# Performance work log

Hardware: AMD Instinct MI355X
Metric: run time of the kernel (lower is better)

Reference implementation:

```python
import jax, jax.numpy as jnp
import numpy as np
import math

B, C, N, T = 8, 128, 256, 64  # batch, d_model, nodes, timesteps
H = 8                          # attention heads
NUM_STEPS = 50                 # diffusion steps


def _conv2d(x, w, b):
    # Conv2d with kernel (1,3), padding (0,1); x: (B,C,N,T), w: (O,I,1,3)
    y = jax.lax.conv_general_dilated(x, w, (1, 1), [(0, 0), (1, 1)],
                                     dimension_numbers=('NCHW', 'OIHW', 'NCHW'))
    return y + b[None, :, None, None]


def _linear(x, w, b=None):
    y = jnp.einsum('...i,oi->...o', x, w)
    return y if b is None else y + b


def _ln(x, g, b, eps=1e-5):
    m = jnp.mean(x, -1, keepdims=True)
    v = jnp.var(x, -1, keepdims=True)
    return (x - m) * jax.lax.rsqrt(v + eps) * g + b


def _forward(step, x, adj, wq, bq, wk, bk, w1, b1, w2, b2, theta,
             ln0_g, ln0_b, ln1_g, ln1_b, p1_w, p1_b, p2_w, p2_b,
             dxc_w, dxc_b, dec_w, dec_b, dc1_w, dc1_b, dp2_w, dp2_b):
    dk = C // H
    sq = 1.0 / math.sqrt(dk)
    sc = 1.0 / math.sqrt(C)
    # ---- normalized graph Laplacian: D^{-1/2} A D^{-1/2} (get_laplacian, normalize=True)
    d = jnp.sum(adj, -1) ** -0.5
    Lap = adj * d[:, None] * d[None, :]  # (N,N)
    # ---- temporal attention with conv-derived Q/K (MultiHeadAttentionAwareTemporal)
    q = _conv2d(x, wq, bq).reshape(B, H, dk, N, T).transpose(0, 3, 1, 4, 2)  # (B,N,H,T,dk)
    k = _conv2d(x, wk, bk).reshape(B, H, dk, N, T).transpose(0, 3, 1, 4, 2)
    v = _linear(x.transpose(0, 2, 3, 1), w1, b1).reshape(B, N, T, H, dk).transpose(0, 1, 3, 2, 4)
    p = jax.nn.softmax(jnp.einsum('bnhtd,bnhsd->bnhts', q, k) * sq, axis=-1)
    o = jnp.einsum('bnhts,bnhsd->bnhtd', p, v).transpose(0, 1, 3, 2, 4).reshape(B, N, T, C)
    xp = x.transpose(0, 2, 3, 1) + _ln(_linear(o, w2, b2), ln0_g, ln0_b)  # (B,N,T,C)
    # ---- spatial attention GCN (Spatial_Attention_layer + spatialAttentionGCN)
    xt = xp.transpose(0, 2, 1, 3)  # (B,T,N,C)
    sat = jax.nn.softmax(jnp.einsum('btnf,btmf->btnm', xt, xt) * sc, axis=-1) * sc
    y = jnp.einsum('btnm,btmf->btnf', Lap[None, None] * sat, xt)
    y = jax.nn.relu(_linear(y, theta)).transpose(0, 2, 1, 3)  # (B,N,T,C)
    h = xp + _ln(y, ln1_g, ln1_b)
    # ---- diffusion step embedding (DiffusionEmbedding)
    dim = C // 2
    freqs = 10.0 ** (jnp.arange(dim, dtype=jnp.float32) / (dim - 1) * 4.0)
    tab = jnp.arange(NUM_STEPS, dtype=jnp.float32)[:, None] * freqs[None, :]
    tab = jnp.concatenate([jnp.sin(tab), jnp.cos(tab)], -1)  # (NUM_STEPS, C)
    e = jax.nn.silu(_linear(tab[step], p1_w, p1_b))
    e = jax.nn.silu(_linear(e, p2_w, p2_b))  # (B,C)
    h = h + e[:, None, None, :]
    # ---- Decoder: conv + sigmoid-gated add + relu + 1x1 projection to 2 channels
    enc = h.transpose(0, 3, 1, 2)  # (B,C,N,T)
    xh = _conv2d(enc, dxc_w, dxc_b)
    ec = _conv2d(enc, dec_w, dec_b)
    out = jax.nn.relu(xh + jax.nn.sigmoid(ec) + _conv2d(ec, dc1_w, dc1_b))
    out = jnp.einsum('bcnt,oc->bont', out, dp2_w) + dp2_b[None, :, None, None]  # (B,2,N,T)
    return out


def setup_inputs() -> dict:
    key = jax.random.key(0)
    ks = iter(jax.random.split(key, 40))
    s = 1.0 / math.sqrt(C)
    sk = 1.0 / math.sqrt(3 * C)

    def nrm(shape, scale):
        return jax.random.normal(next(ks), shape, jnp.float32) * scale

    return {
        'x': nrm((B, C, N, T), 1.0),
        'adj': jax.random.uniform(next(ks), (N, N), jnp.float32, 0.1, 1.0),
        'step': jax.random.randint(next(ks), (B,), 0, NUM_STEPS, jnp.int32),
        'wq': nrm((C, C, 1, 3), sk), 'bq': jnp.zeros((C,), jnp.float32),
        'wk': nrm((C, C, 1, 3), sk), 'bk': jnp.zeros((C,), jnp.float32),
        'w1': nrm((C, C), s), 'b1': jnp.zeros((C,), jnp.float32),
        'w2': nrm((C, C), s), 'b2': jnp.zeros((C,), jnp.float32),
        'theta': nrm((C, C), s),
        'ln0_g': jnp.ones((C,), jnp.float32), 'ln0_b': jnp.zeros((C,), jnp.float32),
        'ln1_g': jnp.ones((C,), jnp.float32), 'ln1_b': jnp.zeros((C,), jnp.float32),
        'p1_w': nrm((C, C), s), 'p1_b': jnp.zeros((C,), jnp.float32),
        'p2_w': nrm((C, C), s), 'p2_b': jnp.zeros((C,), jnp.float32),
        'dxc_w': nrm((C, C, 1, 3), sk), 'dxc_b': jnp.zeros((C,), jnp.float32),
        'dec_w': nrm((C, C, 1, 3), sk), 'dec_b': jnp.zeros((C,), jnp.float32),
        'dc1_w': nrm((C, C, 1, 3), sk), 'dc1_b': jnp.zeros((C,), jnp.float32),
        'dp2_w': nrm((2, C), s), 'dp2_b': jnp.zeros((2,), jnp.float32),
    }


def reference(x, adj, step, wq, bq, wk, bk, w1, b1, w2, b2, theta,
              ln0_g, ln0_b, ln1_g, ln1_b, p1_w, p1_b, p2_w, p2_b,
              dxc_w, dxc_b, dec_w, dec_b, dc1_w, dc1_b, dp2_w, dp2_b):
    return _forward(step, x, adj, wq, bq, wk, bk, w1, b1, w2, b2, theta,
                    ln0_g, ln0_b, ln1_g, ln1_b, p1_w, p1_b, p2_w, p2_b,
                    dxc_w, dxc_b, dec_w, dec_b, dc1_w, dc1_b, dp2_w, dp2_b)
```

## Files before the change

### kernel.cpp

```cpp
#include <hip/hip_runtime.h>
#include <hip/hip_bf16.h>

namespace {

constexpr int C = 128, N = 256, T = 64, Bsz = 8;
constexpr int TILE = T * C;
constexpr size_t BIGE = (size_t)Bsz * N * T * C;

typedef short v8s __attribute__((ext_vector_type(8)));
typedef float v4f __attribute__((ext_vector_type(4)));

__device__ __forceinline__ float bfu(unsigned short u) {
  unsigned int x = ((unsigned int)u) << 16;
  return __uint_as_float(x);
}
__device__ __forceinline__ unsigned short f2b(float v) {
  __hip_bfloat16 h = __float2bfloat16(v);
  return *(unsigned short*)&h;
}
__device__ __forceinline__ unsigned int pk2(float a, float b) {
  return (unsigned int)f2b(a) | ((unsigned int)f2b(b) << 16);
}
__device__ __forceinline__ float ld(const void* p, size_t i, int f32) {
  if (f32) return ((const float*)p)[i];
  return bfu(((const unsigned short*)p)[i]);
}
__device__ __forceinline__ float sigm(float x) { return 1.f / (1.f + __expf(-x)); }

__global__ __launch_bounds__(64) void k_sniff(const unsigned short* x, int* flag) {
  __shared__ int cnt[64];
  int tid = threadIdx.x;
  int c = 0;
  for (int u = 0; u < 8; ++u) {
    unsigned short v = x[tid * 8 + u];
    int e = (v >> 7) & 255;
    c += (e >= 97 && e <= 157) ? 1 : 0;
  }
  cnt[tid] = c;
  __syncthreads();
  if (tid == 0) {
    int s = 0;
    for (int i = 0; i < 64; ++i) s += cnt[i];
    flag[0] = (s < 435) ? 1 : 0;
  }
}

__global__ __launch_bounds__(256) void k_dsh(const void* adj, const int* flag, float* dsh) {
  int f = flag[0];
  int row = blockIdx.x * 8 + (threadIdx.x >> 5);
  int l32 = threadIdx.x & 31;
  float s = 0.f;
#pragma unroll
  for (int j = 0; j < 8; ++j) s += ld(adj, (size_t)row * 256 + l32 + j * 32, f);
#pragma unroll
  for (int m = 16; m > 0; m >>= 1) s += __shfl_xor(s, m, 32);
  if (l32 == 0) dsh[row] = 1.f / sqrtf(s);
}

struct PrepArgs {
  const int* flag;
  const void *wq, *wk, *w1, *w2, *th, *dxc, *dec, *dc1;
  const void *bq, *bk, *b1, *b2, *l0g, *l0b, *l1g, *l1b, *dxcb, *decb, *dc1b, *dp2w, *dp2b;
  unsigned short *wqkB, *w1B, *w2B;
  __hip_bfloat16* thB;
  unsigned short *decWb, *dxcWb, *dc1Wb;
  float *bqk, *b1f, *b2f, *l0gf, *l0bf, *l1gf, *l1bf, *dxcbf, *decbf, *dc1bf, *dp2wf, *dp2bf;
};

__global__ __launch_bounds__(256) void k_prepall(
    PrepArgs a, const void* adj, const float* dsh, float* lap, const int* step,
    const void* p1w, const void* p1b, const void* p2w, const void* p2b, float* e) {
  __shared__ float sh[256];
  __shared__ float e1[128];
  int f = a.flag[0];
  int blk = blockIdx.x, tid = threadIdx.x;
  if (blk < 128) {
    int idx = blk * 256 + tid;
    const int stride = 32768;
    for (int i = idx; i < 256 * 384; i += stride) {
      int o = i / 384, k = i - o * 384;
      int j = k >> 7, ii = k & 127;
      float v = (o < 128) ? ld(a.wq, (o * 128 + ii) * 3 + j, f)
                          : ld(a.wk, ((o - 128) * 128 + ii) * 3 + j, f);
      a.wqkB[i] = f2b(v);
    }
    for (int i = idx; i < 16384; i += stride) {
      a.w1B[i] = f2b(ld(a.w1, i, f));
      a.w2B[i] = f2b(ld(a.w2, i, f));
      a.thB[i] = __float2bfloat16(ld(a.th, i, f));
    }
    for (int i = idx; i < 16384; i += stride) {
      int o = i >> 7, ii = i & 127;
      int sbase = (o * 128 + ii) * 3;
#pragma unroll
      for (int j = 0; j < 3; ++j) {
        int dsti = o * 384 + j * 128 + ii;
        a.decWb[dsti] = f2b(ld(a.dec, sbase + j, f));
        a.dxcWb[dsti] = f2b(ld(a.dxc, sbase + j, f));
        a.dc1Wb[dsti] = f2b(ld(a.dc1, sbase + j, f));
      }
    }
    for (int i = idx; i < 256; i += stride) {
      a.bqk[i] = (i < 128) ? ld(a.bq, i, f) : ld(a.bk, i - 128, f);
      a.dp2wf[i] = ld(a.dp2w, i, f);
    }
    for (int i = idx; i < 128; i += stride) {
      a.b1f[i] = ld(a.b1, i, f);   a.b2f[i] = ld(a.b2, i, f);
      a.l0gf[i] = ld(a.l0g, i, f); a.l0bf[i] = ld(a.l0b, i, f);
      a.l1gf[i] = ld(a.l1g, i, f); a.l1bf[i] = ld(a.l1b, i, f);
      a.dxcbf[i] = ld(a.dxcb, i, f); a.decbf[i] = ld(a.decb, i, f); a.dc1bf[i] = ld(a.dc1b, i, f);
    }
    if (idx < 2) a.dp2bf[idx] = ld(a.dp2b, idx, f);
  } else if (blk < 192) {
    int n0 = (blk - 128) * 4;
    for (int idx = tid; idx < 1024; idx += 256) {
      int n = n0 + (idx >> 8), m = idx & 255;
      lap[n * 256 + m] = ld(adj, n * 256 + m, f) * dsh[n] * dsh[m];
    }
  } else {
    int b = blk - 192;
    if (tid < 128) {
      float sv = (float)step[b];
      int i0 = tid & 63;
      float fr = powf(10.f, (float)i0 / 63.f * 4.f);
      float ang = sv * fr;
      sh[tid] = (tid < 64) ? sinf(ang) : cosf(ang);
    }
    __syncthreads();
    if (tid < 128) {
      float aa = ld(p1b, tid, f);
      for (int i = 0; i < 128; ++i) aa += sh[i] * ld(p1w, tid * 128 + i, f);
      aa = aa * sigm(aa);
      e1[tid] = aa;
    }
    __syncthreads();
    if (tid < 128) {
      float a2 = ld(p2b, tid, f);
      for (int i = 0; i < 128; ++i) a2 += e1[i] * ld(p2w, tid * 128 + i, f);
      e[b * 128 + tid] = a2 * sigm(a2);
    }
  }
}

constexpr int XBS = 136;
constexpr int VTS = 72;

__global__ __launch_bounds__(512, 4) void k_mega1(
    const void* xin, const int* flag,
    const unsigned short* wqkB, const float* bqk,
    const unsigned short* w1B, const float* b1f,
    const unsigned short* w2B, const float* b2f,
    const float* l0g, const float* l0b, float* g0) {
  int bn = blockIdx.x, b = bn >> 8, n = bn & 255;
  __shared__ unsigned short Xb[66 * XBS];
  __shared__ unsigned short qo[64 * XBS];
  __shared__ unsigned short kls[64 * XBS];
  __shared__ unsigned short vT[128 * VTS];
  __shared__ float pS[8 * 64], pQ[8 * 64];
  __shared__ float mrow[64], vrow[64];
  int tid = threadIdx.x;
  int wv = tid >> 6, lane = tid & 63, quad = lane >> 4, lr = lane & 15;
  int f = flag[0];
  int hb = wv * 16;
  const v8s zz = {0, 0, 0, 0, 0, 0, 0, 0};
  {
    size_t xoff = (size_t)b * C * N * T + (size_t)n * T;
    const int NT = N * T;
    for (int idx = tid; idx < 1024; idx += 512) {
      int t = idx & 63, c0 = (idx >> 6) * 8;
      union { unsigned short us[8]; uint4 q; } pk;
      if (f) {
        const float* xp = (const float*)xin + xoff + (size_t)c0 * NT + t;
#pragma unroll
        for (int u = 0; u < 8; ++u) pk.us[u] = f2b(xp[(size_t)u * NT]);
      } else {
        const unsigned short* xp = (const unsigned short*)xin + xoff + (size_t)c0 * NT + t;
#pragma unroll
        for (int u = 0; u < 8; ++u) pk.us[u] = xp[(size_t)u * NT];
      }
      *(uint4*)&Xb[(t + 1) * XBS + c0] = pk.q;
    }
    if (tid < 128) { Xb[tid] = 0; Xb[65 * XBS + tid] = 0; }
  }
  __syncthreads();
  {
    int mt0 = wv * 2;
    v4f acc[2][4];
#pragma unroll
    for (int mi = 0; mi < 2; ++mi)
#pragma unroll
      for (int nt = 0; nt < 4; ++nt) acc[mi][nt] = (v4f){0.f, 0.f, 0.f, 0.f};
    for (int j = 0; j < 3; ++j) {
#pragma unroll
      for (int kt = 0; kt < 4; ++kt) {
        int ko = j * 128 + kt * 32 + quad * 8;
        v8s a0 = *(const v8s*)&wqkB[(mt0 * 16 + lr) * 384 + ko];
        v8s a1 = *(const v8s*)&wqkB[((mt0 + 1) * 16 + lr) * 384 + ko];
        int bko = kt * 32 + quad * 8;
#pragma unroll
        for (int nt = 0; nt < 4; ++nt) {
          v8s bb = *(const v8s*)&Xb[(nt * 16 + lr + j) * XBS + bko];
          acc[0][nt] = __builtin_amdgcn_mfma_f32_16x16x32_bf16(a0, bb, acc[0][nt], 0, 0, 0);
          acc[1][nt] = __builtin_amdgcn_mfma_f32_16x16x32_bf16(a1, bb, acc[1][nt], 0, 0, 0);
        }
      }
    }
    unsigned short* dst = (wv < 4) ? qo : kls;
#pragma unroll
    for (int mi = 0; mi < 2; ++mi) {
      int og = (mt0 + mi) * 16 + quad * 4;
      int oo = og & 127;
#pragma unroll
      for (int nt = 0; nt < 4; ++nt) {
        int t = nt * 16 + lr;
        *(unsigned int*)&dst[t * XBS + oo] =
            pk2(acc[mi][nt][0] + bqk[og], acc[mi][nt][1] + bqk[og + 1]);
        *(unsigned int*)&dst[t * XBS + oo + 2] =
            pk2(acc[mi][nt][2] + bqk[og + 2], acc[mi][nt][3] + bqk[og + 3]);
      }
    }
  }
  {
    v4f av[4];
#pragma unroll
    for (int nt = 0; nt < 4; ++nt) av[nt] = (v4f){0.f, 0.f, 0.f, 0.f};
#pragma unroll
    for (int kt = 0; kt < 4; ++kt) {
      int ko = kt * 32 + quad * 8;
      v8s a = *(const v8s*)&w1B[(wv * 16 + lr) * 128 + ko];
#pragma unroll
      for (int nt = 0; nt < 4; ++nt) {
        v8s bb = *(const v8s*)&Xb[(nt * 16 + lr + 1) * XBS + ko];
        av[nt] = __builtin_amdgcn_mfma_f32_16x16x32_bf16(a, bb, av[nt], 0, 0, 0);
      }
    }
#pragma unroll
    for (int nt = 0; nt < 4; ++nt) {
      int t = nt * 16 + lr;
#pragma unroll
      for (int r = 0; r < 4; ++r) {
        int o = hb + quad * 4 + r;
        vT[o * VTS + t] = f2b(av[nt][r] + b1f[o]);
      }
    }
  }
  __syncthreads();
  {
    v4f sa[4][4];
#pragma unroll
    for (int ms = 0; ms < 4; ++ms)
#pragma unroll
      for (int nt = 0; nt < 4; ++nt) sa[ms][nt] = (v4f){0.f, 0.f, 0.f, 0.f};
    {
      v8s afs[4], bfs[4];
#pragma unroll
      for (int ms = 0; ms < 4; ++ms)
        afs[ms] = (quad < 2) ? *(const v8s*)&kls[(ms * 16 + lr) * XBS + hb + quad * 8] : zz;
#pragma unroll
      for (int nt = 0; nt < 4; ++nt)
        bfs[nt] = (quad < 2) ? *(const v8s*)&qo[(nt * 16 + lr) * XBS + hb + quad * 8] : zz;
#pragma unroll
      for (int ms = 0; ms < 4; ++ms)
#pragma unroll
        for (int nt = 0; nt < 4; ++nt)
          sa[ms][nt] = __builtin_amdgcn_mfma_f32_16x16x32_bf16(afs[ms], bfs[nt], sa[ms][nt], 0, 0, 0);
    }
#pragma unroll
    for (int nt = 0; nt < 4; ++nt) {
      float mx = -1e30f;
#pragma unroll
      for (int ms = 0; ms < 4; ++ms)
#pragma unroll
        for (int r = 0; r < 4; ++r) {
          float v = sa[ms][nt][r] * 0.25f;
          sa[ms][nt][r] = v;
          mx = fmaxf(mx, v);
        }
      mx = fmaxf(mx, __shfl_xor(mx, 16, 64));
      mx = fmaxf(mx, __shfl_xor(mx, 32, 64));
      float ssum = 0.f;
#pragma unroll
      for (int ms = 0; ms < 4; ++ms)
#pragma unroll
        for (int r = 0; r < 4; ++r) {
          float e = __expf(sa[ms][nt][r] - mx);
          sa[ms][nt][r] = e;
          ssum += e;
        }
      ssum += __shfl_xor(ssum, 16, 64);
      ssum += __shfl_xor(ssum, 32, 64);
      float inv = 1.f / ssum;
#pragma unroll
      for (int ms = 0; ms < 4; ++ms)
#pragma unroll
        for (int r = 0; r < 4; ++r) sa[ms][nt][r] *= inv;
    }
    v4f ov[4];
#pragma unroll
    for (int nt = 0; nt < 4; ++nt) ov[nt] = (v4f){0.f, 0.f, 0.f, 0.f};
#pragma unroll
    for (int kt = 0; kt < 2; ++kt) {
      unsigned int pA[4][2], pB[4][2];
#pragma unroll
      for (int nt = 0; nt < 4; ++nt) {
#pragma unroll
        for (int h = 0; h < 2; ++h) {
          pA[nt][h] = pk2(sa[2 * kt][nt][2 * h], sa[2 * kt][nt][2 * h + 1]);
          pB[nt][h] = pk2(sa[2 * kt + 1][nt][2 * h], sa[2 * kt + 1][nt][2 * h + 1]);
        }
      }
      v8s aV = *(const v8s*)&vT[(hb + lr) * VTS + kt * 32 + quad * 8];
#pragma unroll
      for (int nt = 0; nt < 4; ++nt) {
        union { unsigned int u[4]; v8s s; } bu;
#pragma unroll
        for (int w = 0; w < 4; ++w) {
          int src = (2 * (quad & 1) + (w >> 1)) * 16 + lr;
          unsigned int x0 = (unsigned int)__shfl((int)pA[nt][w & 1], src, 64);
          unsigned int x1 = (unsigned int)__shfl((int)pB[nt][w & 1], src, 64);
          bu.u[w] = (quad >> 1) ? x1 : x0;
        }
        ov[nt] = __builtin_amdgcn_mfma_f32_16x16x32_bf16(aV, bu.s, ov[nt], 0, 0, 0);
      }
    }
#pragma unroll
    for (int nt = 0; nt < 4; ++nt) {
      int t = nt * 16 + lr;
      *(unsigned int*)&qo[t * XBS + hb + quad * 4] = pk2(ov[nt][0], ov[nt][1]);
      *(unsigned int*)&qo[t * XBS + hb + quad * 4 + 2] = pk2(ov[nt][2], ov[nt][3]);
    }
  }
  __syncthreads();
  v4f aw[4];
  {
#pragma unroll
    for (int nt = 0; nt < 4; ++nt) aw[nt] = (v4f){0.f, 0.f, 0.f, 0.f};
#pragma unroll
    for (int kt = 0; kt < 4; ++kt) {
      int ko = kt * 32 + quad * 8;
      v8s a = *(const v8s*)&w2B[(wv * 16 + lr) * 128 + ko];
#pragma unroll
      for (int nt = 0; nt < 4; ++nt) {
        v8s bb = *(const v8s*)&qo[(nt * 16 + lr) * XBS + ko];
        aw[nt] = __builtin_amdgcn_mfma_f32_16x16x32_bf16(a, bb, aw[nt], 0, 0, 0);
      }
    }
    int ob = hb + quad * 4;
#pragma unroll
    for (int nt = 0; nt < 4; ++nt) {
      float s = 0.f, q2 = 0.f;
#pragma unroll
      for (int r = 0; r < 4; ++r) {
        aw[nt][r] += b2f[ob + r];
        s += aw[nt][r];
        q2 += aw[nt][r] * aw[nt][r];
      }
      s += __shfl_xor(s, 16, 64);  s += __shfl_xor(s, 32, 64);
      q2 += __shfl_xor(q2, 16, 64); q2 += __shfl_xor(q2, 32, 64);
      if (quad == 0) {
        pS[wv * 64 + nt * 16 + lr] = s;
        pQ[wv * 64 + nt * 16 + lr] = q2;
      }
    }
  }
  __syncthreads();
  if (tid < 64) {
    float s = 0.f, q2 = 0.f;
#pragma unroll
    for (int w = 0; w < 8; ++w) { s += pS[w * 64 + tid]; q2 += pQ[w * 64 + tid]; }
    float mm = s * (1.f / 128.f);
    mrow[tid] = mm;
    vrow[tid] = rsqrtf(q2 * (1.f / 128.f) - mm * mm + 1e-5f);
  }
  __syncthreads();
  {
    int ob = hb + quad * 4;
    float gg[4], bb2[4];
#pragma unroll
    for (int r = 0; r < 4; ++r) { gg[r] = l0g[ob + r]; bb2[r] = l0b[ob + r]; }
    float* dst = g0 + (size_t)bn * TILE;
#pragma unroll
    for (int nt = 0; nt < 4; ++nt) {
      int t = nt * 16 + lr;
      float m = mrow[t], rs = vrow[t];
      ushort4 xr = *(const ushort4*)&Xb[(t + 1) * XBS + ob];
      float4 o4;
      o4.x = (aw[nt][0] - m) * rs * gg[0] + bb2[0] + bfu(xr.x);
      o4.y = (aw[nt][1] - m) * rs * gg[1] + bb2[1] + bfu(xr.y);
      o4.z = (aw[nt][2] - m) * rs * gg[2] + bb2[2] + bfu(xr.z);
      o4.w = (aw[nt][3] - m) * rs * gg[3] + bb2[3] + bfu(xr.w);
      *(float4*)&dst[t * 128 + ob] = o4;
    }
  }
}

constexpr int XS = 136;
constexpr int TS = 264;

__global__ __launch_bounds__(512, 1) void k_megasp(
    const float* g0, const float* lap, const unsigned short* thB,
    const float* l1g, const float* l1b, const float* e, unsigned short* g0b) {
  int bt = blockIdx.x, b = bt >> 6, t = bt & 63;
  __shared__ unsigned short R1[256 * XS];
  __shared__ unsigned short R2[256 * XS];
  unsigned short* Xhi = R1;
  unsigned short* Xlo = R2;
  unsigned short* Xt = R2;
  unsigned short* Pld = R1;
  int tid = threadIdx.x;
  int wv = tid >> 6, lane = tid & 63, quad = lane >> 4, lr = lane & 15;
  int wrow0 = wv * 32;
  const float sc = 0.08838834764831845f;
  {
    size_t base = (size_t)b * (N * (size_t)TILE) + (size_t)t * 128;
    for (int idx = tid * 4; idx < 32768; idx += 2048) {
      int n = idx >> 7, c = idx & 127;
      float4 v4 = *(const float4*)&g0[base + (size_t)n * TILE + c];
      ushort4 h, l;
      h.x = f2b(v4.x); l.x = f2b(v4.x - bfu(h.x));
      h.y = f2b(v4.y); l.y = f2b(v4.y - bfu(h.y));
      h.z = f2b(v4.z); l.z = f2b(v4.z - bfu(h.z));
      h.w = f2b(v4.w); l.w = f2b(v4.w - bfu(h.w));
      *(ushort4*)&Xhi[n * XS + c] = h;
      *(ushort4*)&Xlo[n * XS + c] = l;
    }
  }
  __syncthreads();
  v4f acc[2][16];
#pragma unroll
  for (int mi = 0; mi < 2; ++mi)
#pragma unroll
    for (int nt = 0; nt < 16; ++nt) acc[mi][nt] = (v4f){0.f, 0.f, 0.f, 0.f};
  for (int kt = 0; kt < 4; ++kt) {
    int ko = kt * 32 + quad * 8;
    v8s ah0 = *(const v8s*)&Xhi[(wrow0 + lr) * XS + ko];
    v8s al0 = *(const v8s*)&Xlo[(wrow0 + lr) * XS + ko];
    v8s ah1 = *(const v8s*)&Xhi[(wrow0 + 16 + lr) * XS + ko];
    v8s al1 = *(const v8s*)&Xlo[(wrow0 + 16 + lr) * XS + ko];
#pragma unroll
    for (int nt = 0; nt < 16; ++nt) {
      v8s bh = *(const v8s*)&Xhi[(nt * 16 + lr) * XS + ko];
      v8s bl = *(const v8s*)&Xlo[(nt * 16 + lr) * XS + ko];
      acc[0][nt] = __builtin_amdgcn_mfma_f32_16x16x32_bf16(ah0, bh, acc[0][nt], 0, 0, 0);
      acc[0][nt] = __builtin_amdgcn_mfma_f32_16x16x32_bf16(ah0, bl, acc[0][nt], 0, 0, 0);
      acc[0][nt] = __builtin_amdgcn_mfma_f32_16x16x32_bf16(al0, bh, acc[0][nt], 0, 0, 0);
      acc[1][nt] = __builtin_amdgcn_mfma_f32_16x16x32_bf16(ah1, bh, acc[1][nt], 0, 0, 0);
      acc[1][nt] = __builtin_amdgcn_mfma_f32_16x16x32_bf16(ah1, bl, acc[1][nt], 0, 0, 0);
      acc[1][nt] = __builtin_amdgcn_mfma_f32_16x16x32_bf16(al1, bh, acc[1][nt], 0, 0, 0);
    }
  }
  __syncthreads();
  for (int task = tid; task < 8192; task += 512) {
    int c = task & 127, n0 = (task >> 7) * 4;
    ushort4 w;
    w.x = Xhi[(n0 + 0) * XS + c];
    w.y = Xhi[(n0 + 1) * XS + c];
    w.z = Xhi[(n0 + 2) * XS + c];
    w.w = Xhi[(n0 + 3) * XS + c];
    *(ushort4*)&Xt[c * TS + n0] = w;
  }
  __syncthreads();
  unsigned int pk1[2][8][2];
#pragma unroll
  for (int mi = 0; mi < 2; ++mi) {
#pragma unroll
    for (int r = 0; r < 4; ++r) {
      int row = wrow0 + 16 * mi + quad * 4 + r;
      float mx = -1e30f;
#pragma unroll
      for (int nt = 0; nt < 16; ++nt) {
        acc[mi][nt][r] *= sc;
        mx = fmaxf(mx, acc[mi][nt][r]);
      }
#pragma unroll
      for (int m = 8; m > 0; m >>= 1) mx = fmaxf(mx, __shfl_xor(mx, m, 16));
      float ex[16];
      float ssum = 0.f;
#pragma unroll
      for (int nt = 0; nt < 16; ++nt) { ex[nt] = __expf(acc[mi][nt][r] - mx); ssum += ex[nt]; }
#pragma unroll
      for (int m = 8; m > 0; m >>= 1) ssum += __shfl_xor(ssum, m, 16);
      float inv = sc / ssum;
      const float* lrow = lap + row * 256 + lr;
#pragma unroll
      for (int nt = 0; nt < 8; ++nt)
        Pld[row * XS + nt * 16 + lr] = f2b(ex[nt] * inv * lrow[nt * 16]);
#pragma unroll
      for (int nt = 8; nt < 16; ++nt) {
        unsigned int hbw = (unsigned int)f2b(ex[nt] * inv * lrow[nt * 16]);
        if ((r & 1) == 0) pk1[mi][nt - 8][r >> 1] = hbw;
        else pk1[mi][nt - 8][r >> 1] |= hbw << 16;
      }
    }
  }
  v4f acc2[2][8];
#pragma unroll
  for (int mi = 0; mi < 2; ++mi)
#pragma unroll
    for (int nt = 0; nt < 8; ++nt) acc2[mi][nt] = (v4f){0.f, 0.f, 0.f, 0.f};
#pragma unroll
  for (int h = 0; h < 2; ++h) {
    if (h == 1) {
#pragma unroll
      for (int mi = 0; mi < 2; ++mi) {
        int rowb = wrow0 + 16 * mi + quad * 4;
#pragma unroll
        for (int k = 0; k < 8; ++k) {
          int col = k * 16 + lr;
          unsigned int u0 = pk1[mi][k][0], u1 = pk1[mi][k][1];
          Pld[(rowb + 0) * XS + col] = (unsigned short)u0;
          Pld[(rowb + 1) * XS + col] = (unsigned short)(u0 >> 16);
          Pld[(rowb + 2) * XS + col] = (unsigned short)u1;
          Pld[(rowb + 3) * XS + col] = (unsigned short)(u1 >> 16);
        }
      }
    }
    for (int kt = 0; kt < 4; ++kt) {
      int ko = kt * 32 + quad * 8;
      v8s pa0 = *(const v8s*)&Pld[(wrow0 + lr) * XS + ko];
      v8s pa1 = *(const v8s*)&Pld[(wrow0 + 16 + lr) * XS + ko];
#pragma unroll
      for (int nt = 0; nt < 8; ++nt) {
        v8s xb = *(const v8s*)&Xt[(nt * 16 + lr) * TS + h * 128 + ko];
        acc2[0][nt] = __builtin_amdgcn_mfma_f32_16x16x32_bf16(pa0, xb, acc2[0][nt], 0, 0, 0);
        acc2[1][nt] = __builtin_amdgcn_mfma_f32_16x16x32_bf16(pa1, xb, acc2[1][nt], 0, 0, 0);
      }
    }
  }
  __syncthreads();
  unsigned short* yB = R2;
  unsigned short* ths = R1;
#pragma unroll
  for (int mi = 0; mi < 2; ++mi) {
    int nb = wrow0 + 16 * mi + quad * 4;
#pragma unroll
    for (int nt = 0; nt < 8; ++nt) {
      int c = nt * 16 + lr;
#pragma unroll
      for (int r = 0; r < 4; ++r)
        yB[(nb + r) * XS + c] = f2b(acc2[mi][nt][r]);
    }
  }
  for (int idx = tid * 8; idx < 16384; idx += 4096) {
    int o = idx >> 7, k = idx & 127;
    *(uint4*)&ths[o * 136 + k] = *(const uint4*)&thB[idx];
  }
  __syncthreads();
  v4f acc3[2][8];
#pragma unroll
  for (int nt2 = 0; nt2 < 2; ++nt2)
#pragma unroll
    for (int ot = 0; ot < 8; ++ot) acc3[nt2][ot] = (v4f){0.f, 0.f, 0.f, 0.f};
#pragma unroll
  for (int kt = 0; kt < 4; ++kt) {
    int ko = kt * 32 + quad * 8;
    v8s b0 = *(const v8s*)&yB[((wv * 2 + 0) * 16 + lr) * XS + ko];
    v8s b1 = *(const v8s*)&yB[((wv * 2 + 1) * 16 + lr) * XS + ko];
#pragma unroll
    for (int ot = 0; ot < 8; ++ot) {
      v8s a = *(const v8s*)&ths[(ot * 16 + lr) * 136 + ko];
      acc3[0][ot] = __builtin_amdgcn_mfma_f32_16x16x32_bf16(a, b0, acc3[0][ot], 0, 0, 0);
      acc3[1][ot] = __builtin_amdgcn_mfma_f32_16x16x32_bf16(a, b1, acc3[1][ot], 0, 0, 0);
    }
  }
  float mmv[2], rrv[2];
#pragma unroll
  for (int nt2 = 0; nt2 < 2; ++nt2) {
    float s = 0.f, q2 = 0.f;
#pragma unroll
    for (int ot = 0; ot < 8; ++ot)
#pragma unroll
      for (int r = 0; r < 4; ++r) {
        float v = fmaxf(acc3[nt2][ot][r], 0.f);
        acc3[nt2][ot][r] = v;
        s += v; q2 += v * v;
      }
    s += __shfl_xor(s, 16, 64);  s += __shfl_xor(s, 32, 64);
    q2 += __shfl_xor(q2, 16, 64); q2 += __shfl_xor(q2, 32, 64);
    mmv[nt2] = s * (1.f / 128.f);
    rrv[nt2] = rsqrtf(q2 * (1.f / 128.f) - mmv[nt2] * mmv[nt2] + 1e-5f);
  }
  {
    const float* eb = e + b * 128;
#pragma unroll
    for (int ot = 0; ot < 8; ++ot) {
      int o0 = ot * 16 + quad * 4;
      float gg[4], bb2[4], ev[4];
#pragma unroll
      for (int r = 0; r < 4; ++r) { gg[r] = l1g[o0 + r]; bb2[r] = l1b[o0 + r]; ev[r] = eb[o0 + r]; }
#pragma unroll
      for (int nt2 = 0; nt2 < 2; ++nt2) {
        int n = (wv * 2 + nt2) * 16 + lr;
        float m = mmv[nt2], rs = rrv[nt2];
        size_t ga = ((size_t)(b * 256 + n)) * TILE + (size_t)t * 128 + o0;
        float4 xa = *(const float4*)&g0[ga];
        ushort4 pk;
        pk.x = f2b((acc3[nt2][ot][0] - m) * rs * gg[0] + bb2[0] + xa.x + ev[0]);
        pk.y = f2b((acc3[nt2][ot][1] - m) * rs * gg[1] + bb2[1] + xa.y + ev[1]);
        pk.z = f2b((acc3[nt2][ot][2] - m) * rs * gg[2] + bb2[2] + xa.z + ev[2]);
        pk.w = f2b((acc3[nt2][ot][3] - m) * rs * gg[3] + bb2[3] + xa.w + ev[3]);
        *(ushort4*)&g0b[ga] = pk;
      }
    }
  }
}

__global__ __launch_bounds__(512, 4) void k_megadec(
    const unsigned short* g0b, const unsigned short* decW, const float* decb,
    const unsigned short* dxcW, const float* dxcb,
    const unsigned short* dc1W, const float* dc1b,
    const float* dp2w, const float* dp2b, const int* flag, void* outv) {
  int bn = blockIdx.x, b = bn >> 8, n = bn & 255;
  int f32o = flag[0];
  __shared__ unsigned short Xm[66 * XBS];
  __shared__ unsigned short E2[66 * XBS];
  __shared__ float pb0[8][64], pb1[8][64];
  int tid = threadIdx.x;
  int wv = tid >> 6, lane = tid & 63, quad = lane >> 4, lr = lane & 15;
  int m0 = wv * 16;
  const unsigned short* gp = g0b + (size_t)bn * TILE;
  for (int idx = tid * 8; idx < TILE; idx += 4096) {
    int t = idx >> 7, c = idx & 127;
    *(uint4*)&Xm[(t + 1) * XBS + c] = *(const uint4*)&gp[idx];
  }
  if (tid < 128) {
    Xm[tid] = 0; Xm[65 * XBS + tid] = 0;
    E2[tid] = 0; E2[65 * XBS + tid] = 0;
  }
  __syncthreads();
  v4f acc[4];
  float ecv[4][4];
#pragma unroll
  for (int nt = 0; nt < 4; ++nt) acc[nt] = (v4f){0.f, 0.f, 0.f, 0.f};
  for (int j = 0; j < 3; ++j) {
#pragma unroll
    for (int kt = 0; kt < 4; ++kt) {
      v8s a = *(const v8s*)&decW[(m0 + lr) * 384 + j * 128 + kt * 32 + quad * 8];
      int bko = kt * 32 + quad * 8;
#pragma unroll
      for (int nt = 0; nt < 4; ++nt) {
        v8s bb = *(const v8s*)&Xm[(nt * 16 + lr + j) * XBS + bko];
        acc[nt] = __builtin_amdgcn_mfma_f32_16x16x32_bf16(a, bb, acc[nt], 0, 0, 0);
      }
    }
  }
#pragma unroll
  for (int nt = 0; nt < 4; ++nt) {
    int t = nt * 16 + lr;
    int o = m0 + quad * 4;
    ushort4 pk;
#pragma unroll
    for (int r = 0; r < 4; ++r) {
      float v = acc[nt][r] + decb[o + r];
      ecv[nt][r] = v;
      ((unsigned short*)&pk)[r] = f2b(v);
    }
    *(ushort4*)&E2[(t + 1) * XBS + o] = pk;
  }
  __syncthreads();
  v4f ax[4], ac[4];
#pragma unroll
  for (int nt = 0; nt < 4; ++nt) { ax[nt] = (v4f){0.f,0.f,0.f,0.f}; ac[nt] = (v4f){0.f,0.f,0.f,0.f}; }
  for (int j = 0; j < 3; ++j) {
#pragma unroll
    for (int kt = 0; kt < 4; ++kt) {
      int wo = (m0 + lr) * 384 + j * 128 + kt * 32 + quad * 8;
      v8s a1 = *(const v8s*)&dxcW[wo];
      v8s a2 = *(const v8s*)&dc1W[wo];
      int bko = kt * 32 + quad * 8;
#pragma unroll
      for (int nt = 0; nt < 4; ++nt) {
        int row = (nt * 16 + lr + j) * XBS + bko;
        v8s b1 = *(const v8s*)&Xm[row];
        v8s b2v = *(const v8s*)&E2[row];
        ax[nt] = __builtin_amdgcn_mfma_f32_16x16x32_bf16(a1, b1, ax[nt], 0, 0, 0);
        ac[nt] = __builtin_amdgcn_mfma_f32_16x16x32_bf16(a2, b2v, ac[nt], 0, 0, 0);
      }
    }
  }
#pragma unroll
  for (int nt = 0; nt < 4; ++nt) {
    float p0 = 0.f, p1 = 0.f;
#pragma unroll
    for (int r = 0; r < 4; ++r) {
      int o = m0 + quad * 4 + r;
      float v = fmaxf(ax[nt][r] + dxcb[o] + sigm(ecv[nt][r]) + ac[nt][r] + dc1b[o], 0.f);
      p0 += v * dp2w[o];
      p1 += v * dp2w[128 + o];
    }
    p0 += __shfl_xor(p0, 16, 64); p0 += __shfl_xor(p0, 32, 64);
    p1 += __shfl_xor(p1, 16, 64); p1 += __shfl_xor(p1, 32, 64);
    if (quad == 0) { pb0[wv][nt * 16 + lr] = p0; pb1[wv][nt * 16 + lr] = p1; }
  }
  __syncthreads();
  if (tid < 128) {
    int ch = tid >> 6, t = tid & 63;
    float s = 0.f;
    if (ch == 0) { for (int w = 0; w < 8; ++w) s += pb0[w][t]; s += dp2b[0]; }
    else         { for (int w = 0; w < 8; ++w) s += pb1[w][t]; s += dp2b[1]; }
    size_t oi = ((size_t)(b * 2 + ch) * 256 + n) * 64 + t;
    if (f32o) ((float*)outv)[oi] = s;
    else ((__hip_bfloat16*)outv)[oi] = __float2bfloat16(s);
  }
}

}

extern "C" void kernel_launch(void* const* d_in, const int* in_sizes, int n_in,
                              void* d_out, int out_size, void* d_ws, size_t ws_size,
                              hipStream_t stream) {
  (void)in_sizes; (void)n_in; (void)out_size; (void)ws_size;
  const void* x    = d_in[0];
  const void* adj  = d_in[1];
  const int*  step = (const int*)d_in[2];
  const void* wq   = d_in[3];
  const void* bq   = d_in[4];
  const void* wk   = d_in[5];
  const void* bk   = d_in[6];
  const void* w1   = d_in[7];
  const void* b1   = d_in[8];
  const void* w2   = d_in[9];
  const void* b2   = d_in[10];
  const void* th   = d_in[11];
  const void* l0g  = d_in[12];
  const void* l0b  = d_in[13];
  const void* l1g  = d_in[14];
  const void* l1b  = d_in[15];
  const void* p1w  = d_in[16];
  const void* p1b  = d_in[17];
  const void* p2w  = d_in[18];
  const void* p2b  = d_in[19];
  const void* dxcw = d_in[20];
  const void* dxcb = d_in[21];
  const void* decw = d_in[22];
  const void* decb = d_in[23];
  const void* dc1w = d_in[24];
  const void* dc1b = d_in[25];
  const void* dp2w = d_in[26];
  const void* dp2b = d_in[27];

  float* ws = (float*)d_ws;
  int* flag = (int*)ws;
  float* p = ws + 16;
  float* e     = p; p += 1024;
  float* lap   = p; p += 65536;
  float* dshv  = p; p += 256;
  float* wqkBv = p; p += 49152;
  float* w1Bv  = p; p += 8192;
  float* w2Bv  = p; p += 8192;
  float* thBv  = p; p += 8192;
  float* decWv = p; p += 24576;
  float* dxcWv = p; p += 24576;
  float* dc1Wv = p; p += 24576;
  float* bqk   = p; p += 256;
  float* b1f   = p; p += 128;
  float* b2f   = p; p += 128;
  float* l0gf  = p; p += 128;
  float* l0bf  = p; p += 128;
  float* l1gf  = p; p += 128;
  float* l1bf  = p; p += 128;
  float* dxcbf = p; p += 128;
  float* decbf = p; p += 128;
  float* dc1bf = p; p += 128;
  float* dp2wf = p; p += 256;
  float* dp2bf = p; p += 8;
  size_t off = (size_t)(p - ws);
  off = (off + 127) & ~(size_t)127;
  float* xf = ws + off;
  float* g0 = xf + BIGE;
  unsigned short* g0b = (unsigned short*)xf;

  PrepArgs pa;
  pa.flag = flag;
  pa.wq = wq; pa.wk = wk; pa.w1 = w1; pa.w2 = w2; pa.th = th;
  pa.dxc = dxcw; pa.dec = decw; pa.dc1 = dc1w;
  pa.bq = bq; pa.bk = bk; pa.b1 = b1; pa.b2 = b2;
  pa.l0g = l0g; pa.l0b = l0b; pa.l1g = l1g; pa.l1b = l1b;
  pa.dxcb = dxcb; pa.decb = decb; pa.dc1b = dc1b; pa.dp2w = dp2w; pa.dp2b = dp2b;
  pa.wqkB = (unsigned short*)wqkBv;
  pa.w1B = (unsigned short*)w1Bv;
  pa.w2B = (unsigned short*)w2Bv;
  pa.thB = (__hip_bfloat16*)thBv;
  pa.decWb = (unsigned short*)decWv;
  pa.dxcWb = (unsigned short*)dxcWv;
  pa.dc1Wb = (unsigned short*)dc1Wv;
  pa.bqk = bqk; pa.b1f = b1f; pa.b2f = b2f;
  pa.l0gf = l0gf; pa.l0bf = l0bf; pa.l1gf = l1gf; pa.l1bf = l1bf;
  pa.dxcbf = dxcbf; pa.decbf = decbf; pa.dc1bf = dc1bf; pa.dp2wf = dp2wf; pa.dp2bf = dp2bf;

  k_sniff<<<1, 64, 0, stream>>>((const unsigned short*)x, flag);
  k_dsh<<<32, 256, 0, stream>>>(adj, flag, dshv);
  k_prepall<<<200, 256, 0, stream>>>(pa, adj, dshv, lap, step, p1w, p1b, p2w, p2b, e);

  k_mega1<<<2048, 512, 0, stream>>>(x, flag, (const unsigned short*)wqkBv, bqk,
                                    (const unsigned short*)w1Bv, b1f,
                                    (const unsigned short*)w2Bv, b2f, l0gf, l0bf, g0);
  k_megasp<<<512, 512, 0, stream>>>(g0, lap, (const unsigned short*)thBv,
                                    l1gf, l1bf, e, g0b);
  k_megadec<<<2048, 512, 0, stream>>>(g0b, (const unsigned short*)decWv, decbf,
                                      (const unsigned short*)dxcWv, dxcbf,
                                      (const unsigned short*)dc1Wv, dc1bf,
                                      dp2wf, dp2bf, flag, d_out);
}
```

Measured before the change: 406.4 us.

## Pass Q/K through register shuffles instead of LDS and share Xm loads

New measurement: 400.7 us. About the same (-1.4%).

```diff
diff --git a/kernel.cpp b/kernel.cpp
--- a/kernel.cpp
+++ b/kernel.cpp
@@ -152,9 +152,8 @@
     const unsigned short* w2B, const float* b2f,
     const float* l0g, const float* l0b, float* g0) {
   int bn = blockIdx.x, b = bn >> 8, n = bn & 255;
-  __shared__ unsigned short Xb[66 * XBS];
+  __shared__ unsigned short Xb[65 * XBS];
   __shared__ unsigned short qo[64 * XBS];
-  __shared__ unsigned short kls[64 * XBS];
   __shared__ unsigned short vT[128 * VTS];
   __shared__ float pS[8 * 64], pQ[8 * 64];
   __shared__ float mrow[64], vrow[64];
@@ -162,7 +161,6 @@
   int wv = tid >> 6, lane = tid & 63, quad = lane >> 4, lr = lane & 15;
   int f = flag[0];
   int hb = wv * 16;
-  const v8s zz = {0, 0, 0, 0, 0, 0, 0, 0};
   {
     size_t xoff = (size_t)b * C * N * T + (size_t)n * T;
     const int NT = N * T;
@@ -180,11 +178,11 @@
       }
       *(uint4*)&Xb[(t + 1) * XBS + c0] = pk.q;
     }
-    if (tid < 128) { Xb[tid] = 0; Xb[65 * XBS + tid] = 0; }
-  }
-  __syncthreads();
+    if (tid < 128) Xb[tid] = 0;
+  }
+  __syncthreads();
+  unsigned int pkq[4][2], pkk[4][2];
   {
-    int mt0 = wv * 2;
     v4f acc[2][4];
 #pragma unroll
     for (int mi = 0; mi < 2; ++mi)
@@ -194,29 +192,28 @@
 #pragma unroll
       for (int kt = 0; kt < 4; ++kt) {
         int ko = j * 128 + kt * 32 + quad * 8;
-        v8s a0 = *(const v8s*)&wqkB[(mt0 * 16 + lr) * 384 + ko];
-        v8s a1 = *(const v8s*)&wqkB[((mt0 + 1) * 16 + lr) * 384 + ko];
+        v8s a0 = *(const v8s*)&wqkB[(wv * 16 + lr) * 384 + ko];
+        v8s a1 = *(const v8s*)&wqkB[((8 + wv) * 16 + lr) * 384 + ko];
         int bko = kt * 32 + quad * 8;
 #pragma unroll
         for (int nt = 0; nt < 4; ++nt) {
-          v8s bb = *(const v8s*)&Xb[(nt * 16 + lr + j) * XBS + bko];
+          int rr = nt * 16 + lr + j;
+          rr = (rr == 65) ? 0 : rr;
+          v8s bb = *(const v8s*)&Xb[rr * XBS + bko];
           acc[0][nt] = __builtin_amdgcn_mfma_f32_16x16x32_bf16(a0, bb, acc[0][nt], 0, 0, 0);
           acc[1][nt] = __builtin_amdgcn_mfma_f32_16x16x32_bf16(a1, bb, acc[1][nt], 0, 0, 0);
         }
       }
     }
-    unsigned short* dst = (wv < 4) ? qo : kls;
-#pragma unroll
-    for (int mi = 0; mi < 2; ++mi) {
-      int og = (mt0 + mi) * 16 + quad * 4;
-      int oo = og & 127;
-#pragma unroll
-      for (int nt = 0; nt < 4; ++nt) {
-        int t = nt * 16 + lr;
-        *(unsigned int*)&dst[t * XBS + oo] =
-            pk2(acc[mi][nt][0] + bqk[og], acc[mi][nt][1] + bqk[og + 1]);
-        *(unsigned int*)&dst[t * XBS + oo + 2] =
-            pk2(acc[mi][nt][2] + bqk[og + 2], acc[mi][nt][3] + bqk[og + 3]);
+    int oq = wv * 16 + quad * 4;
+#pragma unroll
+    for (int nt = 0; nt < 4; ++nt) {
+#pragma unroll
+      for (int h = 0; h < 2; ++h) {
+        pkq[nt][h] = pk2(acc[0][nt][2 * h] + bqk[oq + 2 * h],
+                         acc[0][nt][2 * h + 1] + bqk[oq + 2 * h + 1]);
+        pkk[nt][h] = pk2(acc[1][nt][2 * h] + bqk[128 + oq + 2 * h],
+                         acc[1][nt][2 * h + 1] + bqk[128 + oq + 2 * h + 1]);
       }
     }
   }
@@ -244,27 +241,38 @@
       }
     }
   }
-  __syncthreads();
   {
+    int s0 = ((2 * quad) & 3) * 16 + lr;
+    int s1 = ((2 * quad + 1) & 3) * 16 + lr;
+    v8s afs[4], bfs[4];
+#pragma unroll
+    for (int ms = 0; ms < 4; ++ms) {
+      union { unsigned int u[4]; v8s s; } ka, qa;
+      ka.u[0] = (unsigned int)__shfl((int)pkk[ms][0], s0, 64);
+      ka.u[1] = (unsigned int)__shfl((int)pkk[ms][1], s0, 64);
+      ka.u[2] = (unsigned int)__shfl((int)pkk[ms][0], s1, 64);
+      ka.u[3] = (unsigned int)__shfl((int)pkk[ms][1], s1, 64);
+      qa.u[0] = (unsigned int)__shfl((int)pkq[ms][0], s0, 64);
+      qa.u[1] = (unsigned int)__shfl((int)pkq[ms][1], s0, 64);
+      qa.u[2] = (unsigned int)__shfl((int)pkq[ms][0], s1, 64);
+      qa.u[3] = (unsigned int)__shfl((int)pkq[ms][1], s1, 64);
+      if (quad >= 2) {
+        ka.u[0] = ka.u[1] = ka.u[2] = ka.u[3] = 0;
+        qa.u[0] = qa.u[1] = qa.u[2] = qa.u[3] = 0;
+      }
+      afs[ms] = ka.s;
+      bfs[ms] = qa.s;
+    }
     v4f sa[4][4];
 #pragma unroll
     for (int ms = 0; ms < 4; ++ms)
 #pragma unroll
       for (int nt = 0; nt < 4; ++nt) sa[ms][nt] = (v4f){0.f, 0.f, 0.f, 0.f};
-    {
-      v8s afs[4], bfs[4];
-#pragma unroll
-      for (int ms = 0; ms < 4; ++ms)
-        afs[ms] = (quad < 2) ? *(const v8s*)&kls[(ms * 16 + lr) * XBS + hb + quad * 8] : zz;
+#pragma unroll
+    for (int ms = 0; ms < 4; ++ms)
 #pragma unroll
       for (int nt = 0; nt < 4; ++nt)
-        bfs[nt] = (quad < 2) ? *(const v8s*)&qo[(nt * 16 + lr) * XBS + hb + quad * 8] : zz;
-#pragma unroll
-      for (int ms = 0; ms < 4; ++ms)
-#pragma unroll
-        for (int nt = 0; nt < 4; ++nt)
-          sa[ms][nt] = __builtin_amdgcn_mfma_f32_16x16x32_bf16(afs[ms], bfs[nt], sa[ms][nt], 0, 0, 0);
-    }
+        sa[ms][nt] = __builtin_amdgcn_mfma_f32_16x16x32_bf16(afs[ms], bfs[nt], sa[ms][nt], 0, 0, 0);
 #pragma unroll
     for (int nt = 0; nt < 4; ++nt) {
       float mx = -1e30f;
@@ -628,19 +636,22 @@
     E2[tid] = 0; E2[65 * XBS + tid] = 0;
   }
   __syncthreads();
-  v4f acc[4];
+  v4f acc[4], ax[4];
   float ecv[4][4];
 #pragma unroll
-  for (int nt = 0; nt < 4; ++nt) acc[nt] = (v4f){0.f, 0.f, 0.f, 0.f};
+  for (int nt = 0; nt < 4; ++nt) { acc[nt] = (v4f){0.f,0.f,0.f,0.f}; ax[nt] = (v4f){0.f,0.f,0.f,0.f}; }
   for (int j = 0; j < 3; ++j) {
 #pragma unroll
     for (int kt = 0; kt < 4; ++kt) {
-      v8s a = *(const v8s*)&decW[(m0 + lr) * 384 + j * 128 + kt * 32 + quad * 8];
+      int wo = (m0 + lr) * 384 + j * 128 + kt * 32 + quad * 8;
+      v8s aD = *(const v8s*)&decW[wo];
+      v8s aX = *(const v8s*)&dxcW[wo];
       int bko = kt * 32 + quad * 8;
 #pragma unroll
       for (int nt = 0; nt < 4; ++nt) {
         v8s bb = *(const v8s*)&Xm[(nt * 16 + lr + j) * XBS + bko];
-        acc[nt] = __builtin_amdgcn_mfma_f32_16x16x32_bf16(a, bb, acc[nt], 0, 0, 0);
+        acc[nt] = __builtin_amdgcn_mfma_f32_16x16x32_bf16(aD, bb, acc[nt], 0, 0, 0);
+        ax[nt]  = __builtin_amdgcn_mfma_f32_16x16x32_bf16(aX, bb, ax[nt], 0, 0, 0);
       }
     }
   }
@@ -658,22 +669,17 @@
     *(ushort4*)&E2[(t + 1) * XBS + o] = pk;
   }
   __syncthreads();
-  v4f ax[4], ac[4];
-#pragma unroll
-  for (int nt = 0; nt < 4; ++nt) { ax[nt] = (v4f){0.f,0.f,0.f,0.f}; ac[nt] = (v4f){0.f,0.f,0.f,0.f}; }
+  v4f ac[4];
+#pragma unroll
+  for (int nt = 0; nt < 4; ++nt) ac[nt] = (v4f){0.f, 0.f, 0.f, 0.f};
   for (int j = 0; j < 3; ++j) {
 #pragma unroll
     for (int kt = 0; kt < 4; ++kt) {
-      int wo = (m0 + lr) * 384 + j * 128 + kt * 32 + quad * 8;
-      v8s a1 = *(const v8s*)&dxcW[wo];
-      v8s a2 = *(const v8s*)&dc1W[wo];
+      v8s a2 = *(const v8s*)&dc1W[(m0 + lr) * 384 + j * 128 + kt * 32 + quad * 8];
       int bko = kt * 32 + quad * 8;
 #pragma unroll
       for (int nt = 0; nt < 4; ++nt) {
-        int row = (nt * 16 + lr + j) * XBS + bko;
-        v8s b1 = *(const v8s*)&Xm[row];
-        v8s b2v = *(const v8s*)&E2[row];
-        ax[nt] = __builtin_amdgcn_mfma_f32_16x16x32_bf16(a1, b1, ax[nt], 0, 0, 0);
+        v8s b2v = *(const v8s*)&E2[(nt * 16 + lr + j) * XBS + bko];
         ac[nt] = __builtin_amdgcn_mfma_f32_16x16x32_bf16(a2, b2v, ac[nt], 0, 0, 0);
       }
     }
```
